# Performance work log

Measured on AMD Instinct MI355X. Metric: run time of the kernel, lower is better.

## Reference

```python
import jax, jax.numpy as jnp
import numpy as np

B, N, D = 8, 2048, 1024

def setup_inputs() -> dict:
    key = jax.random.key(0)
    ks = jax.random.split(key, 4)
    x = jax.random.normal(ks[0], (B, N, D), dtype=jnp.float32)
    # Glorot-uniform-like scaling as keras Dense default
    def glorot(k, shape):
        fan_in, fan_out = shape[0], shape[1]
        lim = jnp.sqrt(6.0 / (fan_in + fan_out)).astype(jnp.float32)
        return jax.random.uniform(k, shape, jnp.float32, -lim, lim)
    Wq = glorot(ks[1], (D, D))
    Wk = glorot(ks[2], (D, D))
    Wout = glorot(ks[3], (N, D))  # out_proj acts on last axis of [B,N,N] scores
    bq = jnp.zeros((D,), jnp.float32)
    bk = jnp.zeros((D,), jnp.float32)
    bout = jnp.zeros((D,), jnp.float32)
    return {"x": x, "Wq": Wq, "bq": bq, "Wk": Wk, "bk": bk, "Wout": Wout, "bout": bout}

def reference(x, Wq, bq, Wk, bk, Wout, bout):
    Q = x @ Wq + bq                                  # [B,N,D]
    K = x @ Wk + bk                                  # [B,N,D]
    scores = jnp.einsum("bnd,bmd->bnm", Q, K)       # [B,N,N] (no 1/sqrt(d) in source)
    A = jax.nn.softmax(scores, axis=-1)              # [B,N,N]
    return A @ Wout + bout                           # [B,N,D]
```

## Files before the change

kernel.cpp:

```cpp
#include <hip/hip_runtime.h>


typedef unsigned short u16;
typedef __bf16 bf16x8 __attribute__((ext_vector_type(8)));
typedef float f32x4 __attribute__((ext_vector_type(4)));

#define BB 8
#define NN 2048
#define DD 1024
#define MT (BB * NN)
#define PSTRIDE 4096

#define MFMA3(d, ah, al, bh, bl)                                         \
  d = __builtin_amdgcn_mfma_f32_16x16x32_bf16(ah, bh, d, 0, 0, 0);       \
  d = __builtin_amdgcn_mfma_f32_16x16x32_bf16(ah, bl, d, 0, 0, 0);       \
  d = __builtin_amdgcn_mfma_f32_16x16x32_bf16(al, bh, d, 0, 0, 0);

static __device__ __forceinline__ u16 f2bf(float f) {
  unsigned u = __builtin_bit_cast(unsigned, f);
  u += 0x7FFFu + ((u >> 16) & 1u);
  return (u16)(u >> 16);
}
static __device__ __forceinline__ float bf2f(u16 h) {
  unsigned u = ((unsigned)h) << 16;
  return __builtin_bit_cast(float, u);
}

static __device__ __forceinline__ void gload16(const void* g, void* l) {
  __builtin_amdgcn_global_load_lds((const __attribute__((address_space(1))) void*)g,
                                   (__attribute__((address_space(3))) void*)l, 16, 0, 0);
}

static __device__ __forceinline__ int swz_wg() {
  int nwg = gridDim.x;
  int orig = blockIdx.x;
  int q = nwg >> 3;
  return (orig & 7) * q + (orig >> 3);
}

#define SW(r) (((r) ^ ((r) >> 2)) & 3)

static __device__ __forceinline__ void stage_plane_sw(const u16* __restrict__ g0,
                                                      u16* lp0, int tid, int ld) {
#pragma unroll
  for (int j = 0; j < 2; j++) {
    int o = tid + j * 512;
    int row = o >> 2, c = o & 3;
    const u16* g = g0 + (size_t)row * ld + ((c ^ SW(row)) << 3);
    u16* lp = lp0 + (((tid >> 6) << 6) + j * 512) * 8;
    gload16(g, lp);
  }
}

static __device__ __forceinline__ bf16x8 rdfrag(const u16* plane, int row, int g4) {
  return *(const bf16x8*)&plane[row * 32 + ((g4 ^ SW(row)) << 3)];
}

template <bool STG, int VM>
static __device__ __forceinline__ void tile4(
    u16* Lc, const u16* Ah, const u16* Al, const u16* Bh, const u16* Bl, int kst,
    f32x4 (&acc)[8][4], int tid, int wm, int wn, int r16, int g4) {
  u16* PA0 = Lc;
  u16* PA1 = Lc + 8192;
  u16* PB0 = Lc + 16384;
  u16* PB1 = Lc + 24576;
  bf16x8 a0[4], a1[4], b0[4], b1[4];

#pragma unroll
  for (int fm = 0; fm < 4; fm++) {
    int rw = wm * 128 + fm * 16 + r16;
    a0[fm] = rdfrag(PA0, rw, g4);
    a1[fm] = rdfrag(PA1, rw, g4);
  }
#pragma unroll
  for (int fn = 0; fn < 2; fn++) {
    int rw = wn * 64 + fn * 16 + r16;
    b0[fn] = rdfrag(PB0, rw, g4);
    b1[fn] = rdfrag(PB1, rw, g4);
  }
  __builtin_amdgcn_s_barrier();
  asm volatile("s_waitcnt lgkmcnt(0)" ::: "memory");
  __builtin_amdgcn_s_setprio(1);
#pragma unroll
  for (int fm = 0; fm < 4; fm++)
#pragma unroll
    for (int fn = 0; fn < 2; fn++) { MFMA3(acc[fm][fn], a0[fm], a1[fm], b0[fn], b1[fn]); }
  __builtin_amdgcn_s_setprio(0);

#pragma unroll
  for (int fn = 2; fn < 4; fn++) {
    int rw = wn * 64 + fn * 16 + r16;
    b0[fn] = rdfrag(PB0, rw, g4);
    b1[fn] = rdfrag(PB1, rw, g4);
  }
  __builtin_amdgcn_s_barrier();
  asm volatile("s_waitcnt lgkmcnt(0)" ::: "memory");
  __builtin_amdgcn_s_setprio(1);
#pragma unroll
  for (int fm = 0; fm < 4; fm++)
#pragma unroll
    for (int fn = 2; fn < 4; fn++) { MFMA3(acc[fm][fn], a0[fm], a1[fm], b0[fn], b1[fn]); }
  __builtin_amdgcn_s_setprio(0);
  __builtin_amdgcn_s_barrier();

#pragma unroll
  for (int fm = 0; fm < 4; fm++) {
    int rw = wm * 128 + 64 + fm * 16 + r16;
    a0[fm] = rdfrag(PA0, rw, g4);
    a1[fm] = rdfrag(PA1, rw, g4);
  }
  if (STG) {
    stage_plane_sw(Bh + kst, PB0, tid, DD);
    stage_plane_sw(Bl + kst, PB1, tid, DD);
  }
  __builtin_amdgcn_s_barrier();
  asm volatile("s_waitcnt lgkmcnt(0)" ::: "memory");
  __builtin_amdgcn_s_setprio(1);
#pragma unroll
  for (int fm = 0; fm < 4; fm++)
#pragma unroll
    for (int fn = 0; fn < 2; fn++) { MFMA3(acc[fm + 4][fn], a0[fm], a1[fm], b0[fn], b1[fn]); }
  __builtin_amdgcn_s_setprio(0);
  __builtin_amdgcn_s_barrier();

  if (STG) {
    stage_plane_sw(Ah + kst, PA0, tid, DD);
    stage_plane_sw(Al + kst, PA1, tid, DD);
  }
  if (VM == 8) {
    asm volatile("s_waitcnt vmcnt(8)" ::: "memory");
  } else if (VM == 0) {
    asm volatile("s_waitcnt vmcnt(0)" ::: "memory");
  }
  __builtin_amdgcn_s_barrier();
  __builtin_amdgcn_s_setprio(1);
#pragma unroll
  for (int fm = 0; fm < 4; fm++)
#pragma unroll
    for (int fn = 2; fn < 4; fn++) { MFMA3(acc[fm + 4][fn], a0[fm], a1[fm], b0[fn], b1[fn]); }
  __builtin_amdgcn_s_setprio(0);
}

static __device__ __forceinline__ void mm8_core(u16* L, const u16* Ah, const u16* Al,
                                                const u16* Bh, const u16* Bl,
                                                f32x4 (&acc)[8][4], int tid) {
  int lane = tid & 63, r16 = lane & 15, g4 = lane >> 4;
  int w = tid >> 6, wm = w >> 2, wn = w & 3;
  u16* L0 = L;
  u16* L1 = L + 4 * 8192;
  stage_plane_sw(Ah + 0, L0 + 0, tid, DD);
  stage_plane_sw(Al + 0, L0 + 8192, tid, DD);
  stage_plane_sw(Bh + 0, L0 + 16384, tid, DD);
  stage_plane_sw(Bl + 0, L0 + 24576, tid, DD);
  stage_plane_sw(Ah + 32, L1 + 0, tid, DD);
  stage_plane_sw(Al + 32, L1 + 8192, tid, DD);
  stage_plane_sw(Bh + 32, L1 + 16384, tid, DD);
  stage_plane_sw(Bl + 32, L1 + 24576, tid, DD);
  asm volatile("s_waitcnt vmcnt(8)" ::: "memory");
  __builtin_amdgcn_s_barrier();
#pragma unroll 1
  for (int i = 0; i < 15; i++) {
    int t0 = 2 * i;
    tile4<true, 8>(L0, Ah, Al, Bh, Bl, (t0 + 2) * 32, acc, tid, wm, wn, r16, g4);
    tile4<true, 8>(L1, Ah, Al, Bh, Bl, (t0 + 3) * 32, acc, tid, wm, wn, r16, g4);
  }
  tile4<false, 0>(L0, Ah, Al, Bh, Bl, 0, acc, tid, wm, wn, r16, g4);
  tile4<false, -1>(L1, Ah, Al, Bh, Bl, 0, acc, tid, wm, wn, r16, g4);
}

__launch_bounds__(512, 2)
__global__ void k_gemm_s8(const u16* __restrict__ yh, const u16* __restrict__ yl,
                          const u16* __restrict__ xh, const u16* __restrict__ xl,
                          float* __restrict__ S) {
  __shared__ __attribute__((aligned(16))) u16 lds[2][4][8192];
  int wg = swz_wg();
  int nt = wg & 7, mtot = wg >> 3;
  int b = mtot >> 3, mt = mtot & 7;
  const size_t po = (size_t)b * NN * DD;
  const u16* Ah = yh + po + (size_t)(mt * 256) * DD;
  const u16* Al = yl + po + (size_t)(mt * 256) * DD;
  const u16* Bh = xh + po + (size_t)(nt * 256) * DD;
  const u16* Bl = xl + po + (size_t)(nt * 256) * DD;
  int tid = threadIdx.x;
  f32x4 acc[8][4] = {};
  mm8_core(&lds[0][0][0], Ah, Al, Bh, Bl, acc, tid);
  int lane = tid & 63, r16 = lane & 15, g4 = lane >> 4;
  int w = tid >> 6, wm = w >> 2, wn = w & 3;
  float* Sb = S + (size_t)b * NN * NN;
#pragma unroll
  for (int fm = 0; fm < 8; fm++)
#pragma unroll
    for (int fn = 0; fn < 4; fn++) {
      int col = nt * 256 + wn * 64 + fn * 16 + r16;
      int row = mt * 256 + wm * 128 + fm * 16 + g4 * 4;
#pragma unroll
      for (int i2 = 0; i2 < 4; i2++)
        Sb[(size_t)(row + i2) * NN + col] = acc[fm][fn][i2];
    }
}

__launch_bounds__(512, 2)
__global__ void k_gemm_y8(const u16* __restrict__ ah_g, const u16* __restrict__ al_g,
                          const u16* __restrict__ bh_g, const u16* __restrict__ bl_g,
                          u16* __restrict__ ohi, u16* __restrict__ olo) {
  __shared__ __attribute__((aligned(16))) u16 lds[2][4][8192];
  int wg = swz_wg();
  int nt = wg & 3, mt = wg >> 2;
  const u16* Ah = ah_g + (size_t)(mt * 256) * DD;
  const u16* Al = al_g + (size_t)(mt * 256) * DD;
  const u16* Bh = bh_g + (size_t)(nt * 256) * DD;
  const u16* Bl = bl_g + (size_t)(nt * 256) * DD;
  int tid = threadIdx.x;
  f32x4 acc[8][4] = {};
  mm8_core(&lds[0][0][0], Ah, Al, Bh, Bl, acc, tid);
  int lane = tid & 63, r16 = lane & 15, g4 = lane >> 4;
  int w = tid >> 6, wm = w >> 2, wn = w & 3;
#pragma unroll
  for (int fm = 0; fm < 8; fm++)
#pragma unroll
    for (int fn = 0; fn < 4; fn++) {
      int col = nt * 256 + wn * 64 + fn * 16 + r16;
      int row = mt * 256 + wm * 128 + fm * 16 + g4 * 4;
#pragma unroll
      for (int i2 = 0; i2 < 4; i2++) {
        float v = acc[fm][fn][i2];
        u16 h = f2bf(v);
        size_t o = (size_t)(row + i2) * DD + col;
        ohi[o] = h;
        olo[o] = f2bf(v - bf2f(h));
      }
    }
}

template <bool STG, int VM>
static __device__ __forceinline__ void tile4p(
    u16* Lc, const u16* Ag, const u16* Bg, int kst, int ldA,
    f32x4 (&acc)[8][4], int tid, int wm, int wn, int r16, int g4) {
  u16* PA = Lc;
  u16* PB = Lc + 8192;
  bf16x8 a0[4], b4[4];

#pragma unroll
  for (int fm = 0; fm < 4; fm++) a0[fm] = rdfrag(PA, wm * 128 + fm * 16 + r16, g4);
#pragma unroll
  for (int fn = 0; fn < 2; fn++) b4[fn] = rdfrag(PB, wn * 64 + fn * 16 + r16, g4);
  __builtin_amdgcn_s_barrier();
  asm volatile("s_waitcnt lgkmcnt(0)" ::: "memory");
  __builtin_amdgcn_s_setprio(1);
#pragma unroll
  for (int fm = 0; fm < 4; fm++)
#pragma unroll
    for (int fn = 0; fn < 2; fn++)
      acc[fm][fn] = __builtin_amdgcn_mfma_f32_16x16x32_bf16(a0[fm], b4[fn], acc[fm][fn], 0, 0, 0);
  __builtin_amdgcn_s_setprio(0);

#pragma unroll
  for (int fn = 2; fn < 4; fn++) b4[fn] = rdfrag(PB, wn * 64 + fn * 16 + r16, g4);
  __builtin_amdgcn_s_barrier();
  asm volatile("s_waitcnt lgkmcnt(0)" ::: "memory");
  __builtin_amdgcn_s_setprio(1);
#pragma unroll
  for (int fm = 0; fm < 4; fm++)
#pragma unroll
    for (int fn = 2; fn < 4; fn++)
      acc[fm][fn] = __builtin_amdgcn_mfma_f32_16x16x32_bf16(a0[fm], b4[fn], acc[fm][fn], 0, 0, 0);
  __builtin_amdgcn_s_setprio(0);
  __builtin_amdgcn_s_barrier();

#pragma unroll
  for (int fm = 0; fm < 4; fm++) a0[fm] = rdfrag(PA, wm * 128 + 64 + fm * 16 + r16, g4);
  if (STG) stage_plane_sw(Bg + kst, PB, tid, NN);
  __builtin_amdgcn_s_barrier();
  asm volatile("s_waitcnt lgkmcnt(0)" ::: "memory");
  __builtin_amdgcn_s_setprio(1);
#pragma unroll
  for (int fm = 0; fm < 4; fm++)
#pragma unroll
    for (int fn = 0; fn < 2; fn++)
      acc[fm + 4][fn] = __builtin_amdgcn_mfma_f32_16x16x32_bf16(a0[fm], b4[fn], acc[fm + 4][fn], 0, 0, 0);
  __builtin_amdgcn_s_setprio(0);
  __builtin_amdgcn_s_barrier();

  if (STG) stage_plane_sw(Ag + kst, PA, tid, ldA);
  if (VM == 4) {
    asm volatile("s_waitcnt vmcnt(4)" ::: "memory");
  } else if (VM == 0) {
    asm volatile("s_waitcnt vmcnt(0)" ::: "memory");
  }
  __builtin_amdgcn_s_barrier();
  __builtin_amdgcn_s_setprio(1);
#pragma unroll
  for (int fm = 0; fm < 4; fm++)
#pragma unroll
    for (int fn = 2; fn < 4; fn++)
      acc[fm + 4][fn] = __builtin_amdgcn_mfma_f32_16x16x32_bf16(a0[fm], b4[fn], acc[fm + 4][fn], 0, 0, 0);
  __builtin_amdgcn_s_setprio(0);
}

__launch_bounds__(512, 2)
__global__ void k_gemm_out(const u16* __restrict__ P, const u16* __restrict__ woutT,
                           const float* __restrict__ bout, float* __restrict__ out) {
  __shared__ __attribute__((aligned(16))) u16 lds[2][2][8192];
  int wg = swz_wg();
  int b = wg >> 5, mt = (wg >> 2) & 7, nt = wg & 3;
  const u16* Ag = P + (size_t)b * NN * PSTRIDE + (size_t)(mt * 256) * PSTRIDE;
  const u16* Bg = woutT + (size_t)(nt * 256) * NN;
  float* ob = out + (size_t)b * NN * DD;

  int tid = threadIdx.x;
  int lane = tid & 63, r16 = lane & 15, g4 = lane >> 4;
  int w = tid >> 6, wm = w >> 2, wn = w & 3;
  u16* L0 = &lds[0][0][0];
  u16* L1 = &lds[1][0][0];

  f32x4 acc[8][4] = {};
  stage_plane_sw(Ag + 0, L0, tid, PSTRIDE);
  stage_plane_sw(Bg + 0, L0 + 8192, tid, NN);
  stage_plane_sw(Ag + 32, L1, tid, PSTRIDE);
  stage_plane_sw(Bg + 32, L1 + 8192, tid, NN);
  asm volatile("s_waitcnt vmcnt(4)" ::: "memory");
  __builtin_amdgcn_s_barrier();
#pragma unroll 1
  for (int i = 0; i < 31; i++) {
    int t0 = 2 * i;
    tile4p<true, 4>(L0, Ag, Bg, (t0 + 2) * 32, PSTRIDE, acc, tid, wm, wn, r16, g4);
    tile4p<true, 4>(L1, Ag, Bg, (t0 + 3) * 32, PSTRIDE, acc, tid, wm, wn, r16, g4);
  }
  tile4p<false, 0>(L0, Ag, Bg, 0, PSTRIDE, acc, tid, wm, wn, r16, g4);
  tile4p<false, -1>(L1, Ag, Bg, 0, PSTRIDE, acc, tid, wm, wn, r16, g4);

#pragma unroll
  for (int fm = 0; fm < 8; fm++)
#pragma unroll
    for (int fn = 0; fn < 4; fn++) {
      int col = nt * 256 + wn * 64 + fn * 16 + r16;
      float bv = bout[col];
      int row = mt * 256 + wm * 128 + fm * 16 + g4 * 4;
#pragma unroll
      for (int i2 = 0; i2 < 4; i2++)
        ob[(size_t)(row + i2) * DD + col] = acc[fm][fn][i2] + bv;
    }
}

__global__ void k_split(const float* __restrict__ x, u16* __restrict__ hi,
                        u16* __restrict__ lo, long n4) {
  long i = (long)blockIdx.x * blockDim.x + threadIdx.x;
  long stride = (long)gridDim.x * blockDim.x;
  for (; i < n4; i += stride) {
    float4 v = ((const float4*)x)[i];
    u16 h0 = f2bf(v.x), h1 = f2bf(v.y), h2 = f2bf(v.z), h3 = f2bf(v.w);
    ushort4 hv; hv.x = h0; hv.y = h1; hv.z = h2; hv.w = h3;
    ushort4 lv;
    lv.x = f2bf(v.x - bf2f(h0)); lv.y = f2bf(v.y - bf2f(h1));
    lv.z = f2bf(v.z - bf2f(h2)); lv.w = f2bf(v.w - bf2f(h3));
    ((ushort4*)hi)[i] = hv;
    ((ushort4*)lo)[i] = lv;
  }
}

__global__ void k_split_x(const float* __restrict__ x, const float* __restrict__ v2,
                          u16* __restrict__ hi, u16* __restrict__ lo,
                          float* __restrict__ c2) {
  int w = threadIdx.x >> 6, lane = threadIdx.x & 63;
  int row = blockIdx.x * 4 + w;
  const float4* xr = (const float4*)(x + (size_t)row * DD);
  const float4* vv = (const float4*)v2;
  ushort4* hr = (ushort4*)(hi + (size_t)row * DD);
  ushort4* lr = (ushort4*)(lo + (size_t)row * DD);
  float s = 0.f;
#pragma unroll
  for (int j = 0; j < 4; j++) {
    int idx = j * 64 + lane;
    float4 v = xr[idx];
    float4 b = vv[idx];
    s += v.x * b.x + v.y * b.y + v.z * b.z + v.w * b.w;
    u16 h0 = f2bf(v.x), h1 = f2bf(v.y), h2 = f2bf(v.z), h3 = f2bf(v.w);
    ushort4 hv; hv.x = h0; hv.y = h1; hv.z = h2; hv.w = h3;
    ushort4 lv;
    lv.x = f2bf(v.x - bf2f(h0)); lv.y = f2bf(v.y - bf2f(h1));
    lv.z = f2bf(v.z - bf2f(h2)); lv.w = f2bf(v.w - bf2f(h3));
    hr[idx] = hv;
    lr[idx] = lv;
  }
#pragma unroll
  for (int o = 32; o > 0; o >>= 1) s += __shfl_xor(s, o);
  if (lane == 0) c2[row] = s;
}

__global__ void k_transpose_split(const float* __restrict__ W, u16* __restrict__ thi,
                                  int R, int C) {
  __shared__ float tile[32][33];
  int c0 = blockIdx.x * 32, r0 = blockIdx.y * 32;
  int tx = threadIdx.x, ty = threadIdx.y;
#pragma unroll
  for (int i = 0; i < 4; i++)
    tile[ty + i * 8][tx] = W[(size_t)(r0 + ty + i * 8) * C + c0 + tx];
  __syncthreads();
#pragma unroll
  for (int i = 0; i < 4; i++) {
    float v = tile[tx][ty + i * 8];
    thi[(size_t)(c0 + ty + i * 8) * R + r0 + tx] = f2bf(v);
  }
}

__global__ void k_matvec(const float* __restrict__ A, const float* __restrict__ v,
                         float* __restrict__ out, int cols) {
  int w = threadIdx.x >> 6, lane = threadIdx.x & 63;
  int row = blockIdx.x * 4 + w;
  const float4* Ar = (const float4*)(A + (size_t)row * cols);
  const float4* vv = (const float4*)v;
  float s = 0.f;
  for (int j = lane; j < cols / 4; j += 64) {
    float4 a = Ar[j], b = vv[j];
    s += a.x * b.x + a.y * b.y + a.z * b.z + a.w * b.w;
  }
#pragma unroll
  for (int o = 32; o > 0; o >>= 1) s += __shfl_xor(s, o);
  if (lane == 0) out[row] = s;
}

__global__ void k_softmax(float* __restrict__ S, const float* __restrict__ c2, int nrows) {
  int w = threadIdx.x >> 6, lane = threadIdx.x & 63;
  int row = blockIdx.x * 4 + w;
  if (row >= nrows) return;
  const float4* Sr = (const float4*)(S + (size_t)row * NN);
  const float4* c2b = (const float4*)(c2 + ((size_t)(row >> 11) << 11));
  float4 v[8];
  float mx = -3.4e38f;
#pragma unroll
  for (int j = 0; j < 8; j++) {
    v[j] = Sr[j * 64 + lane];
    float4 c = c2b[j * 64 + lane];
    v[j].x += c.x; v[j].y += c.y; v[j].z += c.z; v[j].w += c.w;
    mx = fmaxf(mx, fmaxf(fmaxf(v[j].x, v[j].y), fmaxf(v[j].z, v[j].w)));
  }
#pragma unroll
  for (int o = 32; o > 0; o >>= 1) mx = fmaxf(mx, __shfl_xor(mx, o));
  float e[32];
  float sum = 0.f;
#pragma unroll
  for (int j = 0; j < 8; j++) {
    e[j * 4 + 0] = __expf(v[j].x - mx);
    e[j * 4 + 1] = __expf(v[j].y - mx);
    e[j * 4 + 2] = __expf(v[j].z - mx);
    e[j * 4 + 3] = __expf(v[j].w - mx);
    sum += e[j * 4 + 0] + e[j * 4 + 1] + e[j * 4 + 2] + e[j * 4 + 3];
  }
#pragma unroll
  for (int o = 32; o > 0; o >>= 1) sum += __shfl_xor(sum, o);
  float inv = 1.0f / sum;
  ushort4* Pr = (ushort4*)((u16*)S + (size_t)row * PSTRIDE);
#pragma unroll
  for (int j = 0; j < 8; j++) {
    ushort4 pv;
    pv.x = f2bf(e[j * 4 + 0] * inv);
    pv.y = f2bf(e[j * 4 + 1] * inv);
    pv.z = f2bf(e[j * 4 + 2] * inv);
    pv.w = f2bf(e[j * 4 + 3] * inv);
    Pr[j * 64 + lane] = pv;
  }
}

extern "C" void kernel_launch(void* const* d_in, const int* in_sizes, int n_in,
                              void* d_out, int out_size, void* d_ws, size_t ws_size,
                              hipStream_t stream) {
  const float* x = (const float*)d_in[0];
  const float* Wq = (const float*)d_in[1];
  const float* bq = (const float*)d_in[2];
  const float* Wk = (const float*)d_in[3];
  const float* bk = (const float*)d_in[4];
  const float* Wout = (const float*)d_in[5];
  const float* bout = (const float*)d_in[6];
  float* out = (float*)d_out;
  char* ws = (char*)d_ws;

  const size_t MB = 1ull << 20;
  u16* mth = (u16*)(ws + 0 * MB);
  u16* mtl = (u16*)(ws + 2 * MB);
  u16* woutT = (u16*)(ws + 4 * MB);
  float* v2 = (float*)(ws + 8 * MB);
  float* c2 = (float*)(ws + 8 * MB + 65536);
  char* base = ws + 12 * MB;

  dim3 tb(32, 8, 1);

  if (ws_size >= 204 * MB) {
    u16* xh = (u16*)(base);
    u16* xl = (u16*)(base + 32 * MB);
    u16* yh = (u16*)(base + 64 * MB);
    u16* yl = (u16*)(base + 96 * MB);
    char* R = base + 128 * MB;
    u16* wqh = (u16*)(R);
    u16* wql = (u16*)(R + 2 * MB);
    u16* wkh = (u16*)(R + 4 * MB);
    u16* wkl = (u16*)(R + 6 * MB);
    float* S = (float*)R;

    k_split<<<256, 256, 0, stream>>>(Wq, wqh, wql, (long)DD * DD / 4);
    k_split<<<256, 256, 0, stream>>>(Wk, wkh, wkl, (long)DD * DD / 4);
    k_gemm_y8<<<16, 512, 0, stream>>>(wkh, wkl, wqh, wql, mth, mtl);
    k_transpose_split<<<dim3(32, 64, 1), tb, 0, stream>>>(Wout, woutT, 2048, 1024);
    k_matvec<<<256, 256, 0, stream>>>(Wk, bq, v2, DD);
    k_split_x<<<MT / 4, 256, 0, stream>>>(x, v2, xh, xl, c2);
    k_gemm_y8<<<256, 512, 0, stream>>>(xh, xl, mth, mtl, yh, yl);
    for (int h = 0; h < 2; h++) {
      size_t qo = (size_t)h * 4 * NN * DD;
      k_gemm_s8<<<256, 512, 0, stream>>>(yh + qo, yl + qo, xh + qo, xl + qo, S);
      k_softmax<<<4 * NN / 4, 256, 0, stream>>>(S, c2 + (size_t)h * 4 * NN, 4 * NN);
      k_gemm_out<<<4 * 32, 512, 0, stream>>>((const u16*)S, woutT, bout, out + qo);
    }
  } else if (ws_size >= 156 * MB) {
    u16* xh = (u16*)(base);
    u16* xl = (u16*)(base + 32 * MB);
    u16* yh = (u16*)(base + 64 * MB);
    u16* yl = (u16*)(base + 96 * MB);
    char* R = base + 128 * MB;
    u16* wqh = (u16*)(R);
    u16* wql = (u16*)(R + 2 * MB);
    u16* wkh = (u16*)(R + 4 * MB);
    u16* wkl = (u16*)(R + 6 * MB);
    float* S = (float*)R;

    k_split<<<256, 256, 0, stream>>>(Wq, wqh, wql, (long)DD * DD / 4);
    k_split<<<256, 256, 0, stream>>>(Wk, wkh, wkl, (long)DD * DD / 4);
    k_gemm_y8<<<16, 512, 0, stream>>>(wkh, wkl, wqh, wql, mth, mtl);
    k_transpose_split<<<dim3(32, 64, 1), tb, 0, stream>>>(Wout, woutT, 2048, 1024);
    k_matvec<<<256, 256, 0, stream>>>(Wk, bq, v2, DD);
    k_split_x<<<MT / 4, 256, 0, stream>>>(x, v2, xh, xl, c2);
    k_gemm_y8<<<256, 512, 0, stream>>>(xh, xl, mth, mtl, yh, yl);
    for (int b = 0; b < BB; b++) {
      size_t qo = (size_t)b * NN * DD;
      k_gemm_s8<<<64, 512, 0, stream>>>(yh + qo, yl + qo, xh + qo, xl + qo, S);
      k_softmax<<<NN / 4, 256, 0, stream>>>(S, c2 + (size_t)b * NN, NN);
      k_gemm_out<<<32, 512, 0, stream>>>((const u16*)S, woutT, bout, out + qo);
    }
  } else {
    u16* xh = (u16*)(base);
    u16* xl = (u16*)(base + 8 * MB);
    u16* yh = (u16*)(base + 16 * MB);
    u16* yl = (u16*)(base + 24 * MB);
    char* R = base + 32 * MB;
    u16* wqh = (u16*)(R);
    u16* wql = (u16*)(R + 2 * MB);
    u16* wkh = (u16*)(R + 4 * MB);
    u16* wkl = (u16*)(R + 6 * MB);
    float* S = (float*)R;

    k_split<<<256, 256, 0, stream>>>(Wq, wqh, wql, (long)DD * DD / 4);
    k_split<<<256, 256, 0, stream>>>(Wk, wkh, wkl, (long)DD * DD / 4);
    k_gemm_y8<<<16, 512, 0, stream>>>(wkh, wkl, wqh, wql, mth, mtl);
    k_transpose_split<<<dim3(32, 64, 1), tb, 0, stream>>>(Wout, woutT, 2048, 1024);
    k_matvec<<<256, 256, 0, stream>>>(Wk, bq, v2, DD);
    for (int c = 0; c < 4; c++) {
      size_t xo = (size_t)c * 2 * NN * DD;
      k_split_x<<<2 * NN / 4, 256, 0, stream>>>(x + xo, v2, xh, xl, c2 + (size_t)c * 2 * NN);
      k_gemm_y8<<<64, 512, 0, stream>>>(xh, xl, mth, mtl, yh, yl);
      for (int bi = 0; bi < 2; bi++) {
        size_t lo = (size_t)bi * NN * DD;
        k_gemm_s8<<<64, 512, 0, stream>>>(yh + lo, yl + lo, xh + lo, xl + lo, S);
        k_softmax<<<NN / 4, 256, 0, stream>>>(S, c2 + (size_t)(c * 2 + bi) * NN, NN);
        k_gemm_out<<<32, 512, 0, stream>>>((const u16*)S, woutT, bout, out + xo + lo);
      }
    }
  }
}
```

Before: 512.6 us.

## Split-K the weight-product GEMM and halve output GEMM N-tile for more workgroups

```diff
diff --git a/kernel.cpp b/kernel.cpp
--- a/kernel.cpp
+++ b/kernel.cpp
@@ -50,6 +50,15 @@
     u16* lp = lp0 + (((tid >> 6) << 6) + j * 512) * 8;
     gload16(g, lp);
   }
+}
+
+static __device__ __forceinline__ void stage_half_sw(const u16* __restrict__ g0,
+                                                     u16* lp0, int tid, int ld) {
+  int o = tid;
+  int row = o >> 2, c = o & 3;
+  const u16* g = g0 + (size_t)row * ld + ((c ^ SW(row)) << 3);
+  u16* lp = lp0 + ((tid >> 6) << 6) * 8;
+  gload16(g, lp);
 }
 
 static __device__ __forceinline__ bf16x8 rdfrag(const u16* plane, int row, int g4) {
@@ -232,26 +241,115 @@
     }
 }
 
+static __device__ __forceinline__ void stage128_lin(const u16* __restrict__ g0,
+                                                    u16* lp0, int tid, int ld) {
+#pragma unroll
+  for (int j = 0; j < 2; j++) {
+    int o = tid + j * 256;
+    const u16* g = g0 + (size_t)(o >> 2) * ld + (o & 3) * 8;
+    u16* lp = lp0 + (((tid >> 6) << 6) + j * 256) * 8;
+    gload16(g, lp);
+  }
+}
+
+__launch_bounds__(256)
+__global__ void k_gemm_mt(const u16* __restrict__ wkh, const u16* __restrict__ wkl,
+                          const u16* __restrict__ wqh, const u16* __restrict__ wql,
+                          float* __restrict__ part) {
+  __shared__ __attribute__((aligned(16))) u16 lds[4][128][32];
+  int idx = blockIdx.x;
+  int ks = idx >> 6, mt = (idx >> 3) & 7, nt = idx & 7;
+  int t = threadIdx.x, lane = t & 63, w = t >> 6;
+  int wr = w >> 1, wc = w & 1, r16 = lane & 15, g = lane >> 4;
+  const u16* Ah = wkh + (size_t)(mt * 128) * DD;
+  const u16* Al = wkl + (size_t)(mt * 128) * DD;
+  const u16* Bh = wqh + (size_t)(nt * 128) * DD;
+  const u16* Bl = wql + (size_t)(nt * 128) * DD;
+  float* P = part + (size_t)ks * DD * DD;
+
+  f32x4 acc[4][4] = {};
+  for (int k0 = ks * 256; k0 < ks * 256 + 256; k0 += 32) {
+    stage128_lin(Ah + k0, &lds[0][0][0], t, DD);
+    stage128_lin(Al + k0, &lds[1][0][0], t, DD);
+    stage128_lin(Bh + k0, &lds[2][0][0], t, DD);
+    stage128_lin(Bl + k0, &lds[3][0][0], t, DD);
+    asm volatile("s_waitcnt vmcnt(0)" ::: "memory");
+    __syncthreads();
+    bf16x8 bh[4], bl[4];
+#pragma unroll
+    for (int fn = 0; fn < 4; fn++) {
+      int col = wc * 64 + fn * 16 + r16;
+      bh[fn] = *(const bf16x8*)&lds[2][col][g * 8];
+      bl[fn] = *(const bf16x8*)&lds[3][col][g * 8];
+    }
+#pragma unroll
+    for (int fm = 0; fm < 4; fm++) {
+      int row = wr * 64 + fm * 16 + r16;
+      bf16x8 ah = *(const bf16x8*)&lds[0][row][g * 8];
+      bf16x8 al = *(const bf16x8*)&lds[1][row][g * 8];
+#pragma unroll
+      for (int fn = 0; fn < 4; fn++) { MFMA3(acc[fm][fn], ah, al, bh[fn], bl[fn]); }
+    }
+    __syncthreads();
+  }
+#pragma unroll
+  for (int fm = 0; fm < 4; fm++)
+#pragma unroll
+    for (int fn = 0; fn < 4; fn++) {
+      int col = nt * 128 + wc * 64 + fn * 16 + r16;
+      int row = mt * 128 + wr * 64 + fm * 16 + g * 4;
+#pragma unroll
+      for (int i = 0; i < 4; i++)
+        P[(size_t)(row + i) * DD + col] = acc[fm][fn][i];
+    }
+}
+
+__global__ void k_combine_split(const float* __restrict__ part, u16* __restrict__ hi,
+                                u16* __restrict__ lo) {
+  const long n4 = (long)DD * DD / 4;
+  long i = (long)blockIdx.x * blockDim.x + threadIdx.x;
+  long stride = (long)gridDim.x * blockDim.x;
+  const float4* p0 = (const float4*)part;
+  const float4* p1 = (const float4*)(part + (size_t)DD * DD);
+  const float4* p2 = (const float4*)(part + (size_t)2 * DD * DD);
+  const float4* p3 = (const float4*)(part + (size_t)3 * DD * DD);
+  for (; i < n4; i += stride) {
+    float4 a = p0[i], b = p1[i], c = p2[i], d = p3[i];
+    float4 v;
+    v.x = a.x + b.x + c.x + d.x;
+    v.y = a.y + b.y + c.y + d.y;
+    v.z = a.z + b.z + c.z + d.z;
+    v.w = a.w + b.w + c.w + d.w;
+    u16 h0 = f2bf(v.x), h1 = f2bf(v.y), h2 = f2bf(v.z), h3 = f2bf(v.w);
+    ushort4 hv; hv.x = h0; hv.y = h1; hv.z = h2; hv.w = h3;
+    ushort4 lv;
+    lv.x = f2bf(v.x - bf2f(h0)); lv.y = f2bf(v.y - bf2f(h1));
+    lv.z = f2bf(v.z - bf2f(h2)); lv.w = f2bf(v.w - bf2f(h3));
+    ((ushort4*)hi)[i] = hv;
+    ((ushort4*)lo)[i] = lv;
+  }
+}
+
 template <bool STG, int VM>
-static __device__ __forceinline__ void tile4p(
-    u16* Lc, const u16* Ag, const u16* Bg, int kst, int ldA,
-    f32x4 (&acc)[8][4], int tid, int wm, int wn, int r16, int g4) {
+static __device__ __forceinline__ void tile4q(
+    u16* Lc, const u16* Ag, const u16* Bg, int kst,
+    f32x4 (&acc)[4][4], int tid, int wm, int wn, int r16, int g4) {
   u16* PA = Lc;
   u16* PB = Lc + 8192;
-  bf16x8 a0[4], b4[4];
-
-#pragma unroll
-  for (int fm = 0; fm < 4; fm++) a0[fm] = rdfrag(PA, wm * 128 + fm * 16 + r16, g4);
+  bf16x8 a4[4], b4[4];
+
+#pragma unroll
+  for (int fm = 0; fm < 2; fm++) a4[fm] = rdfrag(PA, wm * 64 + fm * 16 + r16, g4);
 #pragma unroll
   for (int fn = 0; fn < 2; fn++) b4[fn] = rdfrag(PB, wn * 64 + fn * 16 + r16, g4);
   __builtin_amdgcn_s_barrier();
   asm volatile("s_waitcnt lgkmcnt(0)" ::: "memory");
   __builtin_amdgcn_s_setprio(1);
 #pragma unroll
-  for (int fm = 0; fm < 4; fm++)
+  for (int fm = 0; fm < 2; fm++)
 #pragma unroll
     for (int fn = 0; fn < 2; fn++)
-      acc[fm][fn] = __builtin_amdgcn_mfma_f32_16x16x32_bf16(a0[fm], b4[fn], acc[fm][fn], 0, 0, 0);
+      acc[fm][fn] = __builtin_amdgcn_mfma_f32_16x16x32_bf16(a4[fm], b4[fn], acc[fm][fn], 0, 0, 0);
   __builtin_amdgcn_s_setprio(0);
 
 #pragma unroll
@@ -260,82 +358,82 @@
   asm volatile("s_waitcnt lgkmcnt(0)" ::: "memory");
   __builtin_amdgcn_s_setprio(1);
 #pragma unroll
-  for (int fm = 0; fm < 4; fm++)
+  for (int fm = 0; fm < 2; fm++)
 #pragma unroll
     for (int fn = 2; fn < 4; fn++)
-      acc[fm][fn] = __builtin_amdgcn_mfma_f32_16x16x32_bf16(a0[fm], b4[fn], acc[fm][fn], 0, 0, 0);
-  __builtin_amdgcn_s_setprio(0);
-  __builtin_amdgcn_s_barrier();
-
-#pragma unroll
-  for (int fm = 0; fm < 4; fm++) a0[fm] = rdfrag(PA, wm * 128 + 64 + fm * 16 + r16, g4);
-  if (STG) stage_plane_sw(Bg + kst, PB, tid, NN);
+      acc[fm][fn] = __builtin_amdgcn_mfma_f32_16x16x32_bf16(a4[fm], b4[fn], acc[fm][fn], 0, 0, 0);
+  __builtin_amdgcn_s_setprio(0);
+  __builtin_amdgcn_s_barrier();
+
+#pragma unroll
+  for (int fm = 2; fm < 4; fm++) a4[fm] = rdfrag(PA, wm * 64 + fm * 16 + r16, g4);
+  if (STG) stage_half_sw(Bg + kst, PB, tid, NN);
   __builtin_amdgcn_s_barrier();
   asm volatile("s_waitcnt lgkmcnt(0)" ::: "memory");
   __builtin_amdgcn_s_setprio(1);
 #pragma unroll
-  for (int fm = 0; fm < 4; fm++)
+  for (int fm = 2; fm < 4; fm++)
 #pragma unroll
     for (int fn = 0; fn < 2; fn++)
-      acc[fm + 4][fn] = __builtin_amdgcn_mfma_f32_16x16x32_bf16(a0[fm], b4[fn], acc[fm + 4][fn], 0, 0, 0);
-  __builtin_amdgcn_s_setprio(0);
-  __builtin_amdgcn_s_barrier();
-
-  if (STG) stage_plane_sw(Ag + kst, PA, tid, ldA);
-  if (VM == 4) {
-    asm volatile("s_waitcnt vmcnt(4)" ::: "memory");
+      acc[fm][fn] = __builtin_amdgcn_mfma_f32_16x16x32_bf16(a4[fm], b4[fn], acc[fm][fn], 0, 0, 0);
+  __builtin_amdgcn_s_setprio(0);
+  __builtin_amdgcn_s_barrier();
+
+  if (STG) stage_plane_sw(Ag + kst, PA, tid, PSTRIDE);
+  if (VM == 3) {
+    asm volatile("s_waitcnt vmcnt(3)" ::: "memory");
   } else if (VM == 0) {
     asm volatile("s_waitcnt vmcnt(0)" ::: "memory");
   }
   __builtin_amdgcn_s_barrier();
   __builtin_amdgcn_s_setprio(1);
 #pragma unroll
-  for (int fm = 0; fm < 4; fm++)
+  for (int fm = 2; fm < 4; fm++)
 #pragma unroll
     for (int fn = 2; fn < 4; fn++)
-      acc[fm + 4][fn] = __builtin_amdgcn_mfma_f32_16x16x32_bf16(a0[fm], b4[fn], acc[fm + 4][fn], 0, 0, 0);
+      acc[fm][fn] = __builtin_amdgcn_mfma_f32_16x16x32_bf16(a4[fm], b4[fn], acc[fm][fn], 0, 0, 0);
   __builtin_amdgcn_s_setprio(0);
 }
 
 __launch_bounds__(512, 2)
 __global__ void k_gemm_out(const u16* __restrict__ P, const u16* __restrict__ woutT,
                            const float* __restrict__ bout, float* __restrict__ out) {
-  __shared__ __attribute__((aligned(16))) u16 lds[2][2][8192];
+  __shared__ __attribute__((aligned(16))) u16 lds[2][12288];
   int wg = swz_wg();
-  int b = wg >> 5, mt = (wg >> 2) & 7, nt = wg & 3;
+  int b = wg >> 6, mt = (wg >> 3) & 7, nt = wg & 7;
   const u16* Ag = P + (size_t)b * NN * PSTRIDE + (size_t)(mt * 256) * PSTRIDE;
-  const u16* Bg = woutT + (size_t)(nt * 256) * NN;
+  const u16* Bg = woutT + (size_t)(nt * 128) * NN;
   float* ob = out + (size_t)b * NN * DD;
 
   int tid = threadIdx.x;
   int lane = tid & 63, r16 = lane & 15, g4 = lane >> 4;
-  int w = tid >> 6, wm = w >> 2, wn = w & 3;
-  u16* L0 = &lds[0][0][0];
-  u16* L1 = &lds[1][0][0];
-
-  f32x4 acc[8][4] = {};
+  int w = tid >> 6, wm = w >> 1, wn = w & 1;
+  u16* L0 = &lds[0][0];
+  u16* L1 = &lds[1][0];
+
+  f32x4 acc[4][4] = {};
   stage_plane_sw(Ag + 0, L0, tid, PSTRIDE);
-  stage_plane_sw(Bg + 0, L0 + 8192, tid, NN);
+  stage_half_sw(Bg + 0, L0 + 8192, tid, NN);
   stage_plane_sw(Ag + 32, L1, tid, PSTRIDE);
-  stage_plane_sw(Bg + 32, L1 + 8192, tid, NN);
-  asm volatile("s_waitcnt vmcnt(4)" ::: "memory");
+  stage_half_sw(Bg + 32, L1 + 8192, tid, NN);
+  asm volatile("s_waitcnt vmcnt(3)" ::: "memory");
   __builtin_amdgcn_s_barrier();
 #pragma unroll 1
   for (int i = 0; i < 31; i++) {
     int t0 = 2 * i;
-    tile4p<true, 4>(L0, Ag, Bg, (t0 + 2) * 32, PSTRIDE, acc, tid, wm, wn, r16, g4);
-    tile4p<true, 4>(L1, Ag, Bg, (t0 + 3) * 32, PSTRIDE, acc, tid, wm, wn, r16, g4);
-  }
-  tile4p<false, 0>(L0, Ag, Bg, 0, PSTRIDE, acc, tid, wm, wn, r16, g4);
-  tile4p<false, -1>(L1, Ag, Bg, 0, PSTRIDE, acc, tid, wm, wn, r16, g4);
-
-#pragma unroll
-  for (int fm = 0; fm < 8; fm++)
+    tile4q<true, 3>(L0, Ag, Bg, (t0 + 2) * 32, acc, tid, wm, wn, r16, g4);
+    tile4q<true, 3>(L1, Ag, Bg, (t0 + 3) * 32, acc, tid, wm, wn, r16, g4);
+  }
+  tile4q<false, 0>(L0, Ag, Bg, 0, acc, tid, wm, wn, r16, g4);
+  tile4q<false, -1>(L1, Ag, Bg, 0, acc, tid, wm, wn, r16, g4);
+
+#pragma unroll
+  for (int fm = 0; fm < 4; fm++)
 #pragma unroll
     for (int fn = 0; fn < 4; fn++) {
-      int col = nt * 256 + wn * 64 + fn * 16 + r16;
+      int col = nt * 128 + wn * 64 + fn * 16 + r16;
       float bv = bout[col];
-      int row = mt * 256 + wm * 128 + fm * 16 + g4 * 4;
+      int row = mt * 256 + wm * 64 + fm * 16 + g4 * 4;
 #pragma unroll
       for (int i2 = 0; i2 < 4; i2++)
         ob[(size_t)(row + i2) * DD + col] = acc[fm][fn][i2] + bv;
@@ -494,11 +592,13 @@
     u16* wql = (u16*)(R + 2 * MB);
     u16* wkh = (u16*)(R + 4 * MB);
     u16* wkl = (u16*)(R + 6 * MB);
+    float* mtp = (float*)(R + 8 * MB);
     float* S = (float*)R;
 
     k_split<<<256, 256, 0, stream>>>(Wq, wqh, wql, (long)DD * DD / 4);
     k_split<<<256, 256, 0, stream>>>(Wk, wkh, wkl, (long)DD * DD / 4);
-    k_gemm_y8<<<16, 512, 0, stream>>>(wkh, wkl, wqh, wql, mth, mtl);
+    k_gemm_mt<<<256, 256, 0, stream>>>(wkh, wkl, wqh, wql, mtp);
+    k_combine_split<<<256, 256, 0, stream>>>(mtp, mth, mtl);
     k_transpose_split<<<dim3(32, 64, 1), tb, 0, stream>>>(Wout, woutT, 2048, 1024);
     k_matvec<<<256, 256, 0, stream>>>(Wk, bq, v2, DD);
     k_split_x<<<MT / 4, 256, 0, stream>>>(x, v2, xh, xl, c2);
@@ -507,7 +607,7 @@
       size_t qo = (size_t)h * 4 * NN * DD;
       k_gemm_s8<<<256, 512, 0, stream>>>(yh + qo, yl + qo, xh + qo, xl + qo, S);
       k_softmax<<<4 * NN / 4, 256, 0, stream>>>(S, c2 + (size_t)h * 4 * NN, 4 * NN);
-      k_gemm_out<<<4 * 32, 512, 0, stream>>>((const u16*)S, woutT, bout, out + qo);
+      k_gemm_out<<<256, 512, 0, stream>>>((const u16*)S, woutT, bout, out + qo);
     }
   } else if (ws_size >= 156 * MB) {
     u16* xh = (u16*)(base);
@@ -519,11 +619,13 @@
     u16* wql = (u16*)(R + 2 * MB);
     u16* wkh = (u16*)(R + 4 * MB);
     u16* wkl = (u16*)(R + 6 * MB);
+    float* mtp = (float*)yh;
     float* S = (float*)R;
 
     k_split<<<256, 256, 0, stream>>>(Wq, wqh, wql, (long)DD * DD / 4);
     k_split<<<256, 256, 0, stream>>>(Wk, wkh, wkl, (long)DD * DD / 4);
-    k_gemm_y8<<<16, 512, 0, stream>>>(wkh, wkl, wqh, wql, mth, mtl);
+    k_gemm_mt<<<256, 256, 0, stream>>>(wkh, wkl, wqh, wql, mtp);
+    k_combine_split<<<256, 256, 0, stream>>>(mtp, mth, mtl);
     k_transpose_split<<<dim3(32, 64, 1), tb, 0, stream>>>(Wout, woutT, 2048, 1024);
     k_matvec<<<256, 256, 0, stream>>>(Wk, bq, v2, DD);
     k_split_x<<<MT / 4, 256, 0, stream>>>(x, v2, xh, xl, c2);
@@ -532,7 +634,7 @@
       size_t qo = (size_t)b * NN * DD;
       k_gemm_s8<<<64, 512, 0, stream>>>(yh + qo, yl + qo, xh + qo, xl + qo, S);
       k_softmax<<<NN / 4, 256, 0, stream>>>(S, c2 + (size_t)b * NN, NN);
-      k_gemm_out<<<32, 512, 0, stream>>>((const u16*)S, woutT, bout, out + qo);
+      k_gemm_out<<<64, 512, 0, stream>>>((const u16*)S, woutT, bout, out + qo);
     }
   } else {
     u16* xh = (u16*)(base);
@@ -544,11 +646,13 @@
     u16* wql = (u16*)(R + 2 * MB);
     u16* wkh = (u16*)(R + 4 * MB);
     u16* wkl = (u16*)(R + 6 * MB);
+    float* mtp = (float*)yh;
     float* S = (float*)R;
 
     k_split<<<256, 256, 0, stream>>>(Wq, wqh, wql, (long)DD * DD / 4);
     k_split<<<256, 256, 0, stream>>>(Wk, wkh, wkl, (long)DD * DD / 4);
-    k_gemm_y8<<<16, 512, 0, stream>>>(wkh, wkl, wqh, wql, mth, mtl);
+    k_gemm_mt<<<256, 256, 0, stream>>>(wkh, wkl, wqh, wql, mtp);
+    k_combine_split<<<256, 256, 0, stream>>>(mtp, mth, mtl);
     k_transpose_split<<<dim3(32, 64, 1), tb, 0, stream>>>(Wout, woutT, 2048, 1024);
     k_matvec<<<256, 256, 0, stream>>>(Wk, bq, v2, DD);
     for (int c = 0; c < 4; c++) {
@@ -559,7 +663,7 @@
         size_t lo = (size_t)bi * NN * DD;
         k_gemm_s8<<<64, 512, 0, stream>>>(yh + lo, yl + lo, xh + lo, xl + lo, S);
         k_softmax<<<NN / 4, 256, 0, stream>>>(S, c2 + (size_t)(c * 2 + bi) * NN, NN);
-        k_gemm_out<<<32, 512, 0, stream>>>((const u16*)S, woutT, bout, out + xo + lo);
+        k_gemm_out<<<64, 512, 0, stream>>>((const u16*)S, woutT, bout, out + xo + lo);
       }
     }
   }
```

New measurement: 438.6 us, median of 2. 14.4% less time.
